# Optimization experiments

Hardware: AMD Instinct MI355X
Metric: run time of the kernel (lower is better)

## Reference

```python
import jax, jax.numpy as jnp
import numpy as np

E, K, H, I = 8, 2, 768, 1152  # experts, top_k, hidden, intermediate
T = 4096  # total tokens


def setup_inputs() -> dict:
    key = jax.random.key(0)
    ks = jax.random.split(key, 6)
    return {
        "x": jax.random.normal(ks[0], (T, H), jnp.float32),
        "gate_w": jax.random.normal(ks[1], (E, H), jnp.float32) * 0.02,
        "correction_bias": jnp.zeros((E,), jnp.float32),
        "Wi": jax.random.normal(ks[2], (E, H, 2 * I), jnp.float32) * 0.02,
        "Wo": jax.random.normal(ks[3], (E, I, H), jnp.float32) * 0.02,
        "shared_Wi": jax.random.normal(ks[4], (2 * I, H), jnp.float32) * 0.02,
        "shared_Wo": jax.random.normal(ks[5], (H, I), jnp.float32) * 0.02,
    }


def reference(x, gate_w, correction_bias, Wi, Wo, shared_Wi, shared_Wo):
    # ---- shared SwiGLU expert (dropout=0 in eval) ----
    sh = x @ shared_Wi.T                      # (T, 2I)
    s_in, s_gate = sh[:, :I], sh[:, I:]
    shared_out = (jax.nn.silu(s_in) * s_gate) @ shared_Wo.T  # (T, H)

    # ---- sigmoid top-k router with bias correction ----
    logits = jax.nn.sigmoid(x @ gate_w.T)     # (T, E)
    sel = logits + correction_bias
    _, indices = jax.lax.top_k(sel, K)        # (T, K)
    weights = jnp.take_along_axis(logits, indices, axis=-1)  # bias-free scores
    weights = weights / jnp.sum(weights, axis=-1, keepdims=True)

    # combine weight per (expert, token): cw[e, t] = sum_k weights[t,k]*[indices[t,k]==e]
    one_hot = jax.nn.one_hot(indices, E, dtype=x.dtype)      # (T, K, E)
    cw = jnp.einsum("tke,tk->et", one_hot, weights)          # (E, T)

    # ---- experts: SwiGLU per expert, weighted scatter-combine ----
    h = jnp.einsum("th,ehf->etf", x, Wi)      # (E, T, 2I)
    proj, gate = h[..., :I], h[..., I:]
    act = jax.nn.silu(gate) * proj            # (E, T, I)
    act = act * cw[:, :, None]                # fold combine weights before Wo
    expert_out = jnp.einsum("eti,eih->th", act, Wo)          # (T, H)

    return expert_out + shared_out
```

## Files before the change

kernel.cpp:

```cpp
#include <hip/hip_runtime.h>
#include <stdint.h>

#define E_  8
#define H_  768
#define I_  1152
#define T_  4096
#define F2_ (2*I_)

typedef unsigned short u16;
typedef __attribute__((ext_vector_type(8))) __bf16 bf16x8;
typedef __attribute__((ext_vector_type(4))) float floatx4;

typedef const void __attribute__((address_space(1))) as1_void;
typedef void __attribute__((address_space(3))) as3_void;

__device__ __forceinline__ void gld16(void* lds, const void* g) {
  __builtin_amdgcn_global_load_lds((as1_void*)g, (as3_void*)lds, 16, 0, 0);
}

__device__ __forceinline__ u16 f2bf(float f) {
  union { float f; unsigned int i; } v; v.f = f;
  unsigned int r = v.i + 0x7FFF + ((v.i >> 16) & 1);
  return (u16)(r >> 16);
}

#define GATE_BLKS (T_ / 4)
#define CONV_BLKS ((F2_ * H_ + H_ * I_) / 1024)
#define TWI_X (F2_ / 64)
#define TWI_Y (H_ / 64)
#define TWI_BLKS (TWI_X * TWI_Y * E_)
#define TWO_X (H_ / 64)
#define TWO_Y (I_ / 64)
#define TWO_BLKS (TWO_X * TWO_Y * E_)
#define ZOUT_BLKS ((T_ * H_) / 1024)
#define PREP_BLKS (GATE_BLKS + CONV_BLKS + TWI_BLKS + TWO_BLKS + ZOUT_BLKS)

__device__ __forceinline__ void transpose_role(const float* __restrict__ src,
                                               u16* __restrict__ dst,
                                               int R, int C, int xi, int yi, int zi) {
  __shared__ u16 tile[64][68];
  const float* s = src + (long)zi * R * C;
  u16*         d = dst + (long)zi * R * C;
  int r0 = yi * 64, c0 = xi * 64;
  int c4 = (threadIdx.x & 15) * 4;
  int rr = threadIdx.x >> 4;
  #pragma unroll
  for (int k = 0; k < 64; k += 16) {
    float4 v = *(const float4*)(s + (long)(r0 + rr + k) * C + (c0 + c4));
    ushort4 u;
    u.x = f2bf(v.x); u.y = f2bf(v.y); u.z = f2bf(v.z); u.w = f2bf(v.w);
    *(ushort4*)&tile[rr + k][c4] = u;
  }
  __syncthreads();
  int c  = threadIdx.x >> 2;
  int rq = (threadIdx.x & 3) * 4;
  #pragma unroll
  for (int k = 0; k < 64; k += 16) {
    ushort4 u;
    u.x = tile[rq + k + 0][c];
    u.y = tile[rq + k + 1][c];
    u.z = tile[rq + k + 2][c];
    u.w = tile[rq + k + 3][c];
    *(ushort4*)(d + (long)(c0 + c) * R + (r0 + rq + k)) = u;
  }
}

__global__ __launch_bounds__(256)
void prep_all(const float* __restrict__ x, const float* __restrict__ gw,
              const float* __restrict__ bias,
              int* __restrict__ top2e, float* __restrict__ top2w, u16* __restrict__ xb,
              const float* __restrict__ sWi, u16* __restrict__ sWib,
              const float* __restrict__ sWo, u16* __restrict__ sWob,
              const float* __restrict__ Wi, u16* __restrict__ WiT,
              const float* __restrict__ Wo, u16* __restrict__ WoT,
              float* __restrict__ out) {
  int b = blockIdx.x;
  if (b < GATE_BLKS) {
    int t    = b * 4 + (threadIdx.x >> 6);
    int lane = threadIdx.x & 63;
    float acc[E_];
    #pragma unroll
    for (int e = 0; e < E_; e++) acc[e] = 0.f;
    #pragma unroll
    for (int i = 0; i < H_ / 256; i++) {
      int c = i * 256 + lane * 4;
      float4 xv = *(const float4*)(x + (long)t * H_ + c);
      ushort4 u;
      u.x = f2bf(xv.x); u.y = f2bf(xv.y); u.z = f2bf(xv.z); u.w = f2bf(xv.w);
      *(ushort4*)(xb + (long)t * H_ + c) = u;
      #pragma unroll
      for (int e = 0; e < E_; e++) {
        float4 g = *(const float4*)(gw + e * H_ + c);
        acc[e] += xv.x * g.x + xv.y * g.y + xv.z * g.z + xv.w * g.w;
      }
    }
    #pragma unroll
    for (int e = 0; e < E_; e++) {
      #pragma unroll
      for (int s = 32; s > 0; s >>= 1) acc[e] += __shfl_xor(acc[e], s);
    }
    if (lane == 0) {
      float logits[E_], sel[E_];
      #pragma unroll
      for (int e = 0; e < E_; e++) {
        logits[e] = 1.f / (1.f + expf(-acc[e]));
        sel[e]    = logits[e] + bias[e];
      }
      int i0 = 0;
      #pragma unroll
      for (int e = 1; e < E_; e++) if (sel[e] > sel[i0]) i0 = e;
      int i1 = (i0 == 0) ? 1 : 0;
      #pragma unroll
      for (int e = 0; e < E_; e++) if (e != i0 && sel[e] > sel[i1]) i1 = e;
      float w0 = logits[i0], w1 = logits[i1], s = w0 + w1;
      top2e[t * 2 + 0] = i0;  top2w[t * 2 + 0] = w0 / s;
      top2e[t * 2 + 1] = i1;  top2w[t * 2 + 1] = w1 / s;
    }
  } else if (b < GATE_BLKS + CONV_BLKS) {
    int i = ((b - GATE_BLKS) * 256 + threadIdx.x) * 4;
    const int n1 = F2_ * H_;
    const float* s; u16* d;
    if (i < n1) { s = sWi + i; d = sWib + i; }
    else        { s = sWo + (i - n1); d = sWob + (i - n1); }
    float4 v = *(const float4*)s;
    ushort4 u;
    u.x = f2bf(v.x); u.y = f2bf(v.y); u.z = f2bf(v.z); u.w = f2bf(v.w);
    *(ushort4*)d = u;
  } else if (b < GATE_BLKS + CONV_BLKS + TWI_BLKS) {
    int i = b - (GATE_BLKS + CONV_BLKS);
    int xi = i % TWI_X, yi = (i / TWI_X) % TWI_Y, zi = i / (TWI_X * TWI_Y);
    transpose_role(Wi, WiT, H_, F2_, xi, yi, zi);
  } else if (b < GATE_BLKS + CONV_BLKS + TWI_BLKS + TWO_BLKS) {
    int i = b - (GATE_BLKS + CONV_BLKS + TWI_BLKS);
    int xi = i % TWO_X, yi = (i / TWO_X) % TWO_Y, zi = i / (TWO_X * TWO_Y);
    transpose_role(Wo, WoT, I_, H_, xi, yi, zi);
  } else {
    int i = ((b - (GATE_BLKS + CONV_BLKS + TWI_BLKS + TWO_BLKS)) * 256 + threadIdx.x) * 4;
    float4 z; z.x = z.y = z.z = z.w = 0.f;
    *(float4*)(out + i) = z;
  }
}

__global__ void build_lists(const int* __restrict__ top2e, const float* __restrict__ top2w,
                            int* __restrict__ counts, int* __restrict__ offs,
                            int* __restrict__ list, float* __restrict__ wlist) {
  __shared__ int scnt[4][E_];
  __shared__ int sq[4];
  __shared__ int soffs[E_];
  int e = blockIdx.x;
  int tid = threadIdx.x, w = tid >> 6, lane = tid & 63;
  const int Q = (2 * T_) / 4;

  int c8[E_];
  #pragma unroll
  for (int q = 0; q < E_; q++) c8[q] = 0;
  for (int i = tid; i < 2 * T_; i += 256) {
    int v = top2e[i];
    #pragma unroll
    for (int q = 0; q < E_; q++) c8[q] += (v == q);
  }
  int qstart = w * Q;
  int ce = 0;
  for (int i = qstart + lane; i < qstart + Q; i += 64) ce += (top2e[i] == e);
  #pragma unroll
  for (int q = 0; q < E_; q++)
    #pragma unroll
    for (int s = 32; s > 0; s >>= 1) c8[q] += __shfl_xor(c8[q], s);
  #pragma unroll
  for (int s = 32; s > 0; s >>= 1) ce += __shfl_xor(ce, s);
  if (lane == 0) {
    #pragma unroll
    for (int q = 0; q < E_; q++) scnt[w][q] = c8[q];
    sq[w] = ce;
  }
  __syncthreads();
  if (tid == 0) {
    int s = 0;
    #pragma unroll
    for (int q = 0; q < E_; q++) {
      int tot = scnt[0][q] + scnt[1][q] + scnt[2][q] + scnt[3][q];
      soffs[q] = s;
      if (e == 0) { counts[q] = tot; offs[q] = s; }
      s += tot;
    }
    if (e == 0) { counts[8] = T_; offs[8] = 2 * T_; }
  }
  __syncthreads();
  int base = soffs[e];
  #pragma unroll
  for (int w2 = 0; w2 < 4; w2++) if (w2 < w) base += sq[w2];
  unsigned long long lt = (lane == 63) ? (~0ull >> 1) : ((1ull << lane) - 1);
  for (int i0 = qstart; i0 < qstart + Q; i0 += 64) {
    int s = i0 + lane;
    bool m = (top2e[s] == e);
    unsigned long long mask = __ballot(m);
    if (m) {
      int p = base + __popcll(mask & lt);
      list[p]  = s >> 1;
      wlist[p] = top2w[s];
    }
    base += __popcll(mask);
  }
  for (int t = e * (T_ / 8) + tid; t < (e + 1) * (T_ / 8); t += 256) {
    list[2 * T_ + t]  = t;
    wlist[2 * T_ + t] = 1.f;
  }
}

#define PP1 168
__global__ __launch_bounds__(256, 2)
void gemm_act_all(const u16* __restrict__ A, const u16* __restrict__ WiT,
                  const u16* __restrict__ sWib, u16* __restrict__ act,
                  const int* __restrict__ list, const float* __restrict__ wlist,
                  const int* __restrict__ counts, const int* __restrict__ offsets) {
  __shared__ __align__(16) u16 As[128 * 64];
  __shared__ __align__(16) u16 Bs[2][64 * 64];

  int id = blockIdx.x;
  int y  = id / PP1, p = id - y * PP1;
  if (p >= 162) return;
  int z = p / 18, xblk = p - z * 18;

  int cnt = counts[z], off = offsets[z];
  int row0 = y * 128;
  if (row0 >= cnt) return;
  const u16* B = (z == 8) ? sWib : (WiT + (long)z * F2_ * H_);
  int n0 = xblk * 64;

  int tid  = threadIdx.x;
  int lane = tid & 63, wv = tid >> 6;
  int wr   = wv >> 1, wc = wv & 1;
  int half = lane & 15, quad = lane >> 4;

  int rA  = tid >> 3;
  int lc8 = ((tid & 7) ^ (rA & 7)) * 8;
  const u16* ap[4];
  #pragma unroll
  for (int n = 0; n < 4; n++) {
    int rr = min(row0 + rA + n * 32, cnt - 1);
    ap[n] = A + (long)list[off + rr] * H_ + lc8;
  }
  const u16* bp[2][2];
  #pragma unroll
  for (int h = 0; h < 2; h++)
    #pragma unroll
    for (int m = 0; m < 2; m++)
      bp[h][m] = B + (long)(h * I_ + n0 + m * 32 + rA) * H_ + lc8;

  floatx4 acc[2][4][2];
  #pragma unroll
  for (int q = 0; q < 2; q++)
    #pragma unroll
    for (int i = 0; i < 4; i++)
      #pragma unroll
      for (int j = 0; j < 2; j++) acc[q][i][j] = (floatx4)0.f;

  for (int k0 = 0; k0 < H_; k0 += 64) {
    if (k0) __syncthreads();
    #pragma unroll
    for (int n = 0; n < 4; n++) gld16(As + (n * 256 + tid) * 8, ap[n] + k0);
    #pragma unroll
    for (int h = 0; h < 2; h++)
      #pragma unroll
      for (int m = 0; m < 2; m++) gld16(Bs[h] + (m * 256 + tid) * 8, bp[h][m] + k0);
    __syncthreads();
    #pragma unroll
    for (int kk = 0; kk < 2; kk++) {
      int cs = ((kk * 4 + quad) ^ (half & 7)) * 8;
      bf16x8 a[4], bq[2][2];
      #pragma unroll
      for (int i = 0; i < 4; i++)
        a[i] = *(const bf16x8*)(As + (wr * 64 + i * 16 + half) * 64 + cs);
      #pragma unroll
      for (int q = 0; q < 2; q++)
        #pragma unroll
        for (int j = 0; j < 2; j++)
          bq[q][j] = *(const bf16x8*)(Bs[q] + (wc * 32 + j * 16 + half) * 64 + cs);
      #pragma unroll
      for (int i = 0; i < 4; i++)
        #pragma unroll
        for (int q = 0; q < 2; q++)
          #pragma unroll
          for (int j = 0; j < 2; j++)
            acc[q][i][j] = __builtin_amdgcn_mfma_f32_16x16x32_bf16(a[i], bq[q][j], acc[q][i][j], 0, 0, 0);
    }
  }

  bool sh = (z == 8);
  #pragma unroll
  for (int i = 0; i < 4; i++) {
    #pragma unroll
    for (int r = 0; r < 4; r++) {
      int g = row0 + wr * 64 + i * 16 + quad * 4 + r;
      if (g < cnt) {
        float w = wlist[off + g];
        #pragma unroll
        for (int j = 0; j < 2; j++) {
          float va = acc[0][i][j][r];
          float vb = acc[1][i][j][r];
          float zz = sh ? va : vb;
          float o  = sh ? vb : va;
          float sg = zz / (1.f + expf(-zz));
          float v  = sg * o * w;
          int col  = n0 + wc * 32 + j * 16 + half;
          act[(long)(off + g) * I_ + col] = f2bf(v);
        }
      }
    }
  }
}

#define PP2 40
__global__ __launch_bounds__(256, 4)
void gemm_out_all(const u16* __restrict__ A, const u16* __restrict__ WoT,
                  const u16* __restrict__ sWob, float* __restrict__ out,
                  const int* __restrict__ list,
                  const int* __restrict__ counts, const int* __restrict__ offsets) {
  __shared__ __align__(16) u16 As[64 * 64];
  __shared__ __align__(16) u16 Bs[192 * 64];

  int id = blockIdx.x;
  int y  = id / PP2, p = id - y * PP2;
  if (p >= 36) return;
  int z = p / 4, xblk = p - z * 4;

  int cnt = counts[z], off = offsets[z];
  int row0 = y * 64;
  if (row0 >= cnt) return;
  const u16* B = (z == 8) ? sWob : (WoT + (long)z * H_ * I_);
  int n0 = xblk * 192;

  int tid  = threadIdx.x;
  int lane = tid & 63, wv = tid >> 6;
  int wr   = wv >> 1, wc = wv & 1;
  int half = lane & 15, quad = lane >> 4;

  int rA  = tid >> 3;
  int lc8 = ((tid & 7) ^ (rA & 7)) * 8;
  const u16* ap[2];
  #pragma unroll
  for (int n = 0; n < 2; n++) {
    long rr = off + min(row0 + rA + n * 32, cnt - 1);
    ap[n] = A + rr * I_ + lc8;
  }
  const u16* bp[6];
  #pragma unroll
  for (int m = 0; m < 6; m++)
    bp[m] = B + (long)(n0 + m * 32 + rA) * I_ + lc8;

  floatx4 acc[2][6];
  #pragma unroll
  for (int i = 0; i < 2; i++)
    #pragma unroll
    for (int j = 0; j < 6; j++) acc[i][j] = (floatx4)0.f;

  for (int k0 = 0; k0 < I_; k0 += 64) {
    if (k0) __syncthreads();
    #pragma unroll
    for (int n = 0; n < 2; n++) gld16(As + (n * 256 + tid) * 8, ap[n] + k0);
    #pragma unroll
    for (int m = 0; m < 6; m++) gld16(Bs + (m * 256 + tid) * 8, bp[m] + k0);
    __syncthreads();
    #pragma unroll
    for (int kk = 0; kk < 2; kk++) {
      int cs = ((kk * 4 + quad) ^ (half & 7)) * 8;
      bf16x8 a[2], b[6];
      #pragma unroll
      for (int i = 0; i < 2; i++)
        a[i] = *(const bf16x8*)(As + (wr * 32 + i * 16 + half) * 64 + cs);
      #pragma unroll
      for (int j = 0; j < 6; j++)
        b[j] = *(const bf16x8*)(Bs + (wc * 96 + j * 16 + half) * 64 + cs);
      #pragma unroll
      for (int i = 0; i < 2; i++)
        #pragma unroll
        for (int j = 0; j < 6; j++)
          acc[i][j] = __builtin_amdgcn_mfma_f32_16x16x32_bf16(a[i], b[j], acc[i][j], 0, 0, 0);
    }
  }

  #pragma unroll
  for (int i = 0; i < 2; i++) {
    #pragma unroll
    for (int r = 0; r < 4; r++) {
      int g = row0 + wr * 32 + i * 16 + quad * 4 + r;
      if (g < cnt) {
        int token = list[off + g];
        float* orow = out + (long)token * H_;
        #pragma unroll
        for (int j = 0; j < 6; j++) {
          int col = n0 + wc * 96 + j * 16 + half;
          atomicAdd(orow + col, acc[i][j][r]);
        }
      }
    }
  }
}

extern "C" void kernel_launch(void* const* d_in, const int* in_sizes, int n_in,
                              void* d_out, int out_size, void* d_ws, size_t ws_size,
                              hipStream_t stream) {
  const float* x      = (const float*)d_in[0];
  const float* gate_w = (const float*)d_in[1];
  const float* bias   = (const float*)d_in[2];
  const float* Wi     = (const float*)d_in[3];
  const float* Wo     = (const float*)d_in[4];
  const float* sWi    = (const float*)d_in[5];
  const float* sWo    = (const float*)d_in[6];
  float* out          = (float*)d_out;

  char* ws = (char*)d_ws;
  size_t o = 0;
  auto alloc = [&](size_t bytes) -> void* {
    o = (o + 255) & ~(size_t)255;
    void* p = ws + o;
    o += bytes;
    return p;
  };
  u16*   xb    = (u16*)  alloc((size_t)T_ * H_ * 2);
  u16*   sWib  = (u16*)  alloc((size_t)F2_ * H_ * 2);
  u16*   sWob  = (u16*)  alloc((size_t)H_ * I_ * 2);
  u16*   WiT   = (u16*)  alloc((size_t)E_ * F2_ * H_ * 2);
  u16*   WoT   = (u16*)  alloc((size_t)E_ * H_ * I_ * 2);
  u16*   act   = (u16*)  alloc((size_t)3 * T_ * I_ * 2);
  int*   top2e = (int*)  alloc((size_t)T_ * 2 * 4);
  float* top2w = (float*)alloc((size_t)T_ * 2 * 4);
  int*   count = (int*)  alloc(9 * 4);
  int*   offs  = (int*)  alloc(9 * 4);
  int*   list  = (int*)  alloc((size_t)3 * T_ * 4);
  float* wlist = (float*)alloc((size_t)3 * T_ * 4);

  prep_all<<<PREP_BLKS, 256, 0, stream>>>(x, gate_w, bias, top2e, top2w, xb,
                                          sWi, sWib, sWo, sWob, Wi, WiT, Wo, WoT, out);
  build_lists<<<E_, 256, 0, stream>>>(top2e, top2w, count, offs, list, wlist);

  gemm_act_all<<<32 * PP1, 256, 0, stream>>>(xb, WiT, sWib, act, list, wlist, count, offs);
  gemm_out_all<<<64 * PP2, 256, 0, stream>>>(act, WoT, sWob, out, list, count, offs);
}
```

Baseline: 301.4 us.

## Replace atomic scatter with plain stores and a final gather-reduce

The second GEMM no longer does atomicAdd scatter into the output. The shared expert writes its rows directly into out, and routed experts write their rows into a per-slot buffer that reuses the WiT workspace. A new final_reduce kernel gathers the two routed rows per token using a position map recorded in build_lists. The Wo transpose moves out of prep_all into extra blocks of the first GEMM launch, and the output zeroing pass is removed. This trades atomic contention and the zero-fill for an extra buffer write, a read pass and one more launch.

```diff
diff --git a/kernel.cpp b/kernel.cpp
--- a/kernel.cpp
+++ b/kernel.cpp
@@ -22,6 +22,36 @@
   union { float f; unsigned int i; } v; v.f = f;
   unsigned int r = v.i + 0x7FFF + ((v.i >> 16) & 1);
   return (u16)(r >> 16);
+}
+
+__device__ __forceinline__ void transpose_core(u16 (*tile)[68],
+                                               const float* __restrict__ src,
+                                               u16* __restrict__ dst,
+                                               int R, int C, int xi, int yi, int zi) {
+  const float* s = src + (long)zi * R * C;
+  u16*         d = dst + (long)zi * R * C;
+  int r0 = yi * 64, c0 = xi * 64;
+  int c4 = (threadIdx.x & 15) * 4;
+  int rr = threadIdx.x >> 4;
+  #pragma unroll
+  for (int k = 0; k < 64; k += 16) {
+    float4 v = *(const float4*)(s + (long)(r0 + rr + k) * C + (c0 + c4));
+    ushort4 u;
+    u.x = f2bf(v.x); u.y = f2bf(v.y); u.z = f2bf(v.z); u.w = f2bf(v.w);
+    *(ushort4*)&tile[rr + k][c4] = u;
+  }
+  __syncthreads();
+  int c  = threadIdx.x >> 2;
+  int rq = (threadIdx.x & 3) * 4;
+  #pragma unroll
+  for (int k = 0; k < 64; k += 16) {
+    ushort4 u;
+    u.x = tile[rq + k + 0][c];
+    u.y = tile[rq + k + 1][c];
+    u.z = tile[rq + k + 2][c];
+    u.w = tile[rq + k + 3][c];
+    *(ushort4*)(d + (long)(c0 + c) * R + (r0 + rq + k)) = u;
+  }
 }
 
 #define GATE_BLKS (T_ / 4)
@@ -32,38 +62,7 @@
 #define TWO_X (H_ / 64)
 #define TWO_Y (I_ / 64)
 #define TWO_BLKS (TWO_X * TWO_Y * E_)
-#define ZOUT_BLKS ((T_ * H_) / 1024)
-#define PREP_BLKS (GATE_BLKS + CONV_BLKS + TWI_BLKS + TWO_BLKS + ZOUT_BLKS)
-
-__device__ __forceinline__ void transpose_role(const float* __restrict__ src,
-                                               u16* __restrict__ dst,
-                                               int R, int C, int xi, int yi, int zi) {
-  __shared__ u16 tile[64][68];
-  const float* s = src + (long)zi * R * C;
-  u16*         d = dst + (long)zi * R * C;
-  int r0 = yi * 64, c0 = xi * 64;
-  int c4 = (threadIdx.x & 15) * 4;
-  int rr = threadIdx.x >> 4;
-  #pragma unroll
-  for (int k = 0; k < 64; k += 16) {
-    float4 v = *(const float4*)(s + (long)(r0 + rr + k) * C + (c0 + c4));
-    ushort4 u;
-    u.x = f2bf(v.x); u.y = f2bf(v.y); u.z = f2bf(v.z); u.w = f2bf(v.w);
-    *(ushort4*)&tile[rr + k][c4] = u;
-  }
-  __syncthreads();
-  int c  = threadIdx.x >> 2;
-  int rq = (threadIdx.x & 3) * 4;
-  #pragma unroll
-  for (int k = 0; k < 64; k += 16) {
-    ushort4 u;
-    u.x = tile[rq + k + 0][c];
-    u.y = tile[rq + k + 1][c];
-    u.z = tile[rq + k + 2][c];
-    u.w = tile[rq + k + 3][c];
-    *(ushort4*)(d + (long)(c0 + c) * R + (r0 + rq + k)) = u;
-  }
-}
+#define PREP_BLKS (GATE_BLKS + CONV_BLKS + TWI_BLKS)
 
 __global__ __launch_bounds__(256)
 void prep_all(const float* __restrict__ x, const float* __restrict__ gw,
@@ -71,9 +70,8 @@
               int* __restrict__ top2e, float* __restrict__ top2w, u16* __restrict__ xb,
               const float* __restrict__ sWi, u16* __restrict__ sWib,
               const float* __restrict__ sWo, u16* __restrict__ sWob,
-              const float* __restrict__ Wi, u16* __restrict__ WiT,
-              const float* __restrict__ Wo, u16* __restrict__ WoT,
-              float* __restrict__ out) {
+              const float* __restrict__ Wi, u16* __restrict__ WiT) {
+  __shared__ u16 tile[64][68];
   int b = blockIdx.x;
   if (b < GATE_BLKS) {
     int t    = b * 4 + (threadIdx.x >> 6);
@@ -126,24 +124,17 @@
     ushort4 u;
     u.x = f2bf(v.x); u.y = f2bf(v.y); u.z = f2bf(v.z); u.w = f2bf(v.w);
     *(ushort4*)d = u;
-  } else if (b < GATE_BLKS + CONV_BLKS + TWI_BLKS) {
+  } else {
     int i = b - (GATE_BLKS + CONV_BLKS);
     int xi = i % TWI_X, yi = (i / TWI_X) % TWI_Y, zi = i / (TWI_X * TWI_Y);
-    transpose_role(Wi, WiT, H_, F2_, xi, yi, zi);
-  } else if (b < GATE_BLKS + CONV_BLKS + TWI_BLKS + TWO_BLKS) {
-    int i = b - (GATE_BLKS + CONV_BLKS + TWI_BLKS);
-    int xi = i % TWO_X, yi = (i / TWO_X) % TWO_Y, zi = i / (TWO_X * TWO_Y);
-    transpose_role(Wo, WoT, I_, H_, xi, yi, zi);
-  } else {
-    int i = ((b - (GATE_BLKS + CONV_BLKS + TWI_BLKS + TWO_BLKS)) * 256 + threadIdx.x) * 4;
-    float4 z; z.x = z.y = z.z = z.w = 0.f;
-    *(float4*)(out + i) = z;
+    transpose_core(tile, Wi, WiT, H_, F2_, xi, yi, zi);
   }
 }
 
 __global__ void build_lists(const int* __restrict__ top2e, const float* __restrict__ top2w,
                             int* __restrict__ counts, int* __restrict__ offs,
-                            int* __restrict__ list, float* __restrict__ wlist) {
+                            int* __restrict__ list, float* __restrict__ wlist,
+                            int* __restrict__ pos) {
   __shared__ int scnt[4][E_];
   __shared__ int sq[4];
   __shared__ int soffs[E_];
@@ -198,6 +189,7 @@
       int p = base + __popcll(mask & lt);
       list[p]  = s >> 1;
       wlist[p] = top2w[s];
+      pos[s]   = p;
     }
     base += __popcll(mask);
   }
@@ -208,15 +200,23 @@
 }
 
 #define PP1 168
+#define G1_BLKS (32 * PP1)
 __global__ __launch_bounds__(256, 2)
 void gemm_act_all(const u16* __restrict__ A, const u16* __restrict__ WiT,
                   const u16* __restrict__ sWib, u16* __restrict__ act,
                   const int* __restrict__ list, const float* __restrict__ wlist,
-                  const int* __restrict__ counts, const int* __restrict__ offsets) {
+                  const int* __restrict__ counts, const int* __restrict__ offsets,
+                  const float* __restrict__ Wo, u16* __restrict__ WoT) {
   __shared__ __align__(16) u16 As[128 * 64];
   __shared__ __align__(16) u16 Bs[2][64 * 64];
 
   int id = blockIdx.x;
+  if (id >= G1_BLKS) {
+    int i = id - G1_BLKS;
+    int xi = i % TWO_X, yi = (i / TWO_X) % TWO_Y, zi = i / (TWO_X * TWO_Y);
+    transpose_core((u16(*)[68])As, Wo, WoT, I_, H_, xi, yi, zi);
+    return;
+  }
   int y  = id / PP1, p = id - y * PP1;
   if (p >= 162) return;
   int z = p / 18, xblk = p - z * 18;
@@ -314,7 +314,7 @@
 __global__ __launch_bounds__(256, 4)
 void gemm_out_all(const u16* __restrict__ A, const u16* __restrict__ WoT,
                   const u16* __restrict__ sWob, float* __restrict__ out,
-                  const int* __restrict__ list,
+                  float* __restrict__ eobuf,
                   const int* __restrict__ counts, const int* __restrict__ offsets) {
   __shared__ __align__(16) u16 As[64 * 64];
   __shared__ __align__(16) u16 Bs[192 * 64];
@@ -379,22 +379,34 @@
     }
   }
 
+  bool sh = (z == 8);
   #pragma unroll
   for (int i = 0; i < 2; i++) {
     #pragma unroll
     for (int r = 0; r < 4; r++) {
       int g = row0 + wr * 32 + i * 16 + quad * 4 + r;
       if (g < cnt) {
-        int token = list[off + g];
-        float* orow = out + (long)token * H_;
+        float* orow = sh ? (out + (long)g * H_) : (eobuf + (long)(off + g) * H_);
         #pragma unroll
         for (int j = 0; j < 6; j++) {
           int col = n0 + wc * 96 + j * 16 + half;
-          atomicAdd(orow + col, acc[i][j][r]);
+          orow[col] = acc[i][j][r];
         }
       }
     }
   }
+}
+
+__global__ void final_reduce(float* __restrict__ out, const float* __restrict__ eobuf,
+                             const int* __restrict__ pos) {
+  int gid = blockIdx.x * 256 + threadIdx.x;
+  int t = gid / (H_ / 4), c = (gid % (H_ / 4)) * 4;
+  int p0 = pos[t * 2], p1 = pos[t * 2 + 1];
+  float4 a = *(const float4*)(out   + (long)t  * H_ + c);
+  float4 b = *(const float4*)(eobuf + (long)p0 * H_ + c);
+  float4 d = *(const float4*)(eobuf + (long)p1 * H_ + c);
+  a.x += b.x + d.x; a.y += b.y + d.y; a.z += b.z + d.z; a.w += b.w + d.w;
+  *(float4*)(out + (long)t * H_ + c) = a;
 }
 
 extern "C" void kernel_launch(void* const* d_in, const int* in_sizes, int n_in,
@@ -429,11 +441,15 @@
   int*   offs  = (int*)  alloc(9 * 4);
   int*   list  = (int*)  alloc((size_t)3 * T_ * 4);
   float* wlist = (float*)alloc((size_t)3 * T_ * 4);
+  int*   pos   = (int*)  alloc((size_t)2 * T_ * 4);
+  float* eobuf = (float*)WiT;
 
   prep_all<<<PREP_BLKS, 256, 0, stream>>>(x, gate_w, bias, top2e, top2w, xb,
-                                          sWi, sWib, sWo, sWob, Wi, WiT, Wo, WoT, out);
-  build_lists<<<E_, 256, 0, stream>>>(top2e, top2w, count, offs, list, wlist);
-
-  gemm_act_all<<<32 * PP1, 256, 0, stream>>>(xb, WiT, sWib, act, list, wlist, count, offs);
-  gemm_out_all<<<64 * PP2, 256, 0, stream>>>(act, WoT, sWob, out, list, count, offs);
-}
+                                          sWi, sWib, sWo, sWob, Wi, WiT);
+  build_lists<<<E_, 256, 0, stream>>>(top2e, top2w, count, offs, list, wlist, pos);
+
+  gemm_act_all<<<G1_BLKS + TWO_BLKS, 256, 0, stream>>>(xb, WiT, sWib, act, list, wlist,
+                                                       count, offs, Wo, WoT);
+  gemm_out_all<<<64 * PP2, 256, 0, stream>>>(act, WoT, sWob, out, eobuf, count, offs);
+  final_reduce<<<(T_ * (H_ / 4)) / 256, 256, 0, stream>>>(out, eobuf, pos);
+}
```

Result: faster. 291.7 us (median of 3 runs) (-3.2%).
